# Kernel tuning notes

Measured on AMD Instinct MI355X. Metric: run time of the kernel, lower is better.

The kernel has to match this reference:

```python
import jax, jax.numpy as jnp
import numpy as np

S = 14
B = 2
L_COORD = 5.0
L_NOOBJ = 0.5
NUM_CLS = 20


def setup_inputs() -> dict:
    key = jax.random.key(0)
    k1, k2, k3, k4 = jax.random.split(key, 4)
    N = 4096
    pred_tensor = jax.random.uniform(k1, (N, S, S, B * 5 + NUM_CLS), dtype=jnp.float32)
    target_boxes = jax.random.uniform(k2, (N, S, S, 4), dtype=jnp.float32)
    target_cls = jax.random.uniform(k3, (N, S, S, NUM_CLS), dtype=jnp.float32)
    has_object_map = jax.random.randint(k4, (N, S, S), 0, 2) > 0
    return {"pred_tensor": pred_tensor, "target_boxes": target_boxes,
            "target_cls": target_cls, "has_object_map": has_object_map}


def _xywh2xyxy(b):
    # b[..., 4] in (x, y, w, h); x,y are scaled by S (grid coords)
    x, y, w, h = b[..., 0], b[..., 1], b[..., 2], b[..., 3]
    return jnp.stack([x / S - 0.5 * w, y / S - 0.5 * h,
                      x / S + 0.5 * w, y / S + 0.5 * h], axis=-1)


def reference(pred_tensor, target_boxes, target_cls, has_object_map):
    N = pred_tensor.shape[0]
    maskf = has_object_map.astype(pred_tensor.dtype)  # (N,S,S)

    # split predictions: (N,S,S,B,5) boxes and (N,S,S,20) classes
    pred_boxes = pred_tensor[..., : 5 * B].reshape(pred_tensor.shape[:3] + (B, 5))
    pred_cls = pred_tensor[..., -NUM_CLS:]

    # class loss over object cells
    cls_loss = jnp.sum(((pred_cls - target_cls) ** 2) * maskf[..., None]) / N

    # no-object confidence loss over non-object cells, all B boxes
    no_obj_loss = L_NOOBJ * jnp.sum((pred_boxes[..., 4] ** 2) * (1.0 - maskf)[..., None]) / N

    # IoU of each of the B predicted boxes vs the GT box, per cell (vectorized)
    pb = _xywh2xyxy(pred_boxes[..., :4])              # (N,S,S,B,4)
    gb = _xywh2xyxy(target_boxes)[..., None, :]        # (N,S,S,1,4)
    lt = jnp.maximum(pb[..., :2], gb[..., :2])
    rb = jnp.minimum(pb[..., 2:], gb[..., 2:])
    wh = jnp.clip(rb - lt, 0.0)
    inter = wh[..., 0] * wh[..., 1]                    # (N,S,S,B)
    area_p = (pb[..., 2] - pb[..., 0]) * (pb[..., 3] - pb[..., 1])
    area_g = (gb[..., 2] - gb[..., 0]) * (gb[..., 3] - gb[..., 1])
    iou = inter / (area_p + area_g - inter)            # (N,S,S,B)

    # per-cell best box (first-max index, matching torch.max)
    best_idx = jnp.argmax(iou, axis=-1)                # (N,S,S)
    best_boxes = jnp.take_along_axis(pred_boxes, best_idx[..., None, None], axis=3)
    best_boxes = jnp.squeeze(best_boxes, axis=3)       # (N,S,S,5)

    xy_term = jnp.sum((best_boxes[..., :2] - target_boxes[..., :2]) ** 2, axis=-1)
    wh_term = jnp.sum((jnp.sqrt(best_boxes[..., 2:4]) - jnp.sqrt(target_boxes[..., 2:4])) ** 2, axis=-1)
    reg_loss = L_COORD * jnp.sum((xy_term + wh_term) * maskf) / N

    # containing-object confidence loss: (conf - 1)^2 over object cells
    contain_conf_loss = jnp.sum(((best_boxes[..., 4] - 1.0) ** 2) * maskf) / N

    total_loss = reg_loss + contain_conf_loss + no_obj_loss + cls_loss
    return (total_loss, reg_loss, contain_conf_loss, no_obj_loss, cls_loss)
```

## Files before the change

kernel.cpp:

```cpp
#include <hip/hip_runtime.h>

#define SS 14
#define NUM_CLS 20
#define L_COORD 5.0f
#define L_NOOBJ 0.5f
#define CPB 256


__global__ void __launch_bounds__(256) yolo_main(
    const float* __restrict__ pred,
    const float* __restrict__ tbox,
    const float* __restrict__ tcls,
    const int* __restrict__ mask,
    float4* __restrict__ part) {
  __shared__ float lp[CPB * 30];
  __shared__ float lm[CPB];
  __shared__ float4 red[4];

  const int tid = threadIdx.x;
  const size_t base = (size_t)blockIdx.x * CPB;

  const float4* gc = (const float4*)(tcls + base * 20);
  float4 c0 = gc[tid];
  float4 c1 = gc[tid + 256];
  float4 c2 = gc[tid + 512];
  float4 c3 = gc[tid + 768];
  float4 c4 = gc[tid + 1024];
  float4 tb = ((const float4*)tbox)[base + tid];
  float m = mask[base + tid] ? 1.0f : 0.0f;
  lm[tid] = m;

  const float4* gp = (const float4*)(pred + base * 30);
  float4* sp = (float4*)lp;
#pragma unroll
  for (int i = 0; i < 7; ++i) sp[tid + i * 256] = gp[tid + i * 256];
  if (tid < 128) sp[tid + 1792] = gp[tid + 1792];
  __syncthreads();

  float cls_c = 0.f;
#define CLSQ(cq, i)                                          \
  {                                                          \
    int e = tid + 256 * (i);                                 \
    int cell = e / 5;                                        \
    int k = e - 5 * cell;                                    \
    const float* P = lp + cell * 30 + 10 + 4 * k;            \
    float w = lm[cell];                                      \
    float d0 = P[0] - cq.x, d1 = P[1] - cq.y;                \
    float d2 = P[2] - cq.z, d3 = P[3] - cq.w;                \
    cls_c += w * (d0 * d0 + d1 * d1 + d2 * d2 + d3 * d3);    \
  }
  CLSQ(c0, 0)
  CLSQ(c1, 1)
  CLSQ(c2, 2)
  CLSQ(c3, 3)
  CLSQ(c4, 4)
#undef CLSQ

  const float* P = lp + tid * 30;
  float p0 = P[0], p1 = P[1], p2 = P[2], p3 = P[3], p4 = P[4];
  float p5 = P[5], p6 = P[6], p7 = P[7], p8 = P[8], p9 = P[9];

  float noobj_c = (1.0f - m) * (p4 * p4 + p9 * p9);

  const float invS = 1.0f / (float)SS;
  float gx0 = tb.x * invS - 0.5f * tb.z, gy0 = tb.y * invS - 0.5f * tb.w;
  float gx1 = tb.x * invS + 0.5f * tb.z, gy1 = tb.y * invS + 0.5f * tb.w;
  float ag = (gx1 - gx0) * (gy1 - gy0);

  float iou0, iou1;
  {
    float px0 = p0 * invS - 0.5f * p2, py0 = p1 * invS - 0.5f * p3;
    float px1 = p0 * invS + 0.5f * p2, py1 = p1 * invS + 0.5f * p3;
    float lx = fmaxf(px0, gx0), ly = fmaxf(py0, gy0);
    float rx = fminf(px1, gx1), ry = fminf(py1, gy1);
    float iw = fmaxf(rx - lx, 0.f), ih = fmaxf(ry - ly, 0.f);
    float inter = iw * ih;
    float ap = (px1 - px0) * (py1 - py0);
    iou0 = inter / (ap + ag - inter);
  }
  {
    float px0 = p5 * invS - 0.5f * p7, py0 = p6 * invS - 0.5f * p8;
    float px1 = p5 * invS + 0.5f * p7, py1 = p6 * invS + 0.5f * p8;
    float lx = fmaxf(px0, gx0), ly = fmaxf(py0, gy0);
    float rx = fminf(px1, gx1), ry = fminf(py1, gy1);
    float iw = fmaxf(rx - lx, 0.f), ih = fmaxf(ry - ly, 0.f);
    float inter = iw * ih;
    float ap = (px1 - px0) * (py1 - py0);
    iou1 = inter / (ap + ag - inter);
  }
  bool pick1 = (iou1 > iou0);
  float bx = pick1 ? p5 : p0;
  float by = pick1 ? p6 : p1;
  float bw = pick1 ? p7 : p2;
  float bh = pick1 ? p8 : p3;
  float bc = pick1 ? p9 : p4;

  float dx = bx - tb.x, dy = by - tb.y;
  float dw = sqrtf(bw) - sqrtf(tb.z);
  float dh = sqrtf(bh) - sqrtf(tb.w);
  float reg_c = m * (dx * dx + dy * dy + dw * dw + dh * dh);
  float dc = bc - 1.0f;
  float con_c = m * dc * dc;

  float vx = cls_c, vy = noobj_c, vz = reg_c, vw = con_c;
  for (int off = 32; off >= 1; off >>= 1) {
    vx += __shfl_down(vx, off);
    vy += __shfl_down(vy, off);
    vz += __shfl_down(vz, off);
    vw += __shfl_down(vw, off);
  }
  int wid = tid >> 6;
  if ((tid & 63) == 0) red[wid] = make_float4(vx, vy, vz, vw);
  __syncthreads();
  if (tid == 0) {
    float4 t = red[0];
#pragma unroll
    for (int i = 1; i < 4; ++i) {
      t.x += red[i].x;
      t.y += red[i].y;
      t.z += red[i].z;
      t.w += red[i].w;
    }
    part[blockIdx.x] = t;
  }
}

__global__ void __launch_bounds__(256) yolo_reduce(
    const float4* __restrict__ part, float* __restrict__ out,
    int nblocks, float invN) {
  const int tid = threadIdx.x;
  float vx = 0.f, vy = 0.f, vz = 0.f, vw = 0.f;
  for (int i = tid; i < nblocks; i += 256) {
    float4 t = part[i];
    vx += t.x;
    vy += t.y;
    vz += t.z;
    vw += t.w;
  }
  for (int off = 32; off >= 1; off >>= 1) {
    vx += __shfl_down(vx, off);
    vy += __shfl_down(vy, off);
    vz += __shfl_down(vz, off);
    vw += __shfl_down(vw, off);
  }
  __shared__ float4 red[4];
  int wid = tid >> 6;
  if ((tid & 63) == 0) red[wid] = make_float4(vx, vy, vz, vw);
  __syncthreads();
  if (tid == 0) {
    float4 t = red[0];
#pragma unroll
    for (int i = 1; i < 4; ++i) {
      t.x += red[i].x;
      t.y += red[i].y;
      t.z += red[i].z;
      t.w += red[i].w;
    }
    float cls = t.x * invN;
    float noobj = L_NOOBJ * t.y * invN;
    float reg = L_COORD * t.z * invN;
    float con = t.w * invN;
    out[0] = reg + con + noobj + cls;
    out[1] = reg;
    out[2] = con;
    out[3] = noobj;
    out[4] = cls;
  }
}

extern "C" void kernel_launch(void* const* d_in, const int* in_sizes, int n_in,
                              void* d_out, int out_size, void* d_ws, size_t ws_size,
                              hipStream_t stream) {
  const float* pred = (const float*)d_in[0];
  const float* tbox = (const float*)d_in[1];
  const float* tcls = (const float*)d_in[2];
  const int* mask = (const int*)d_in[3];
  float* out = (float*)d_out;
  float4* part = (float4*)d_ws;

  int ncells = in_sizes[3];
  int nblocks = ncells / CPB;
  float invN = 1.0f / (float)(ncells / (SS * SS));

  yolo_main<<<nblocks, CPB, 0, stream>>>(pred, tbox, tcls, mask, part);
  yolo_reduce<<<1, 256, 0, stream>>>(part, out, nblocks, invN);
}
```

Baseline: 203.4 us.

## Load per-cell predictions directly from global memory instead of staging in LDS

Drops the shared-memory staging of the 30-float prediction rows and the class-loss redistribution. Each thread now reads its own cell's predictions (as float2) and target classes (as float4) straight from global memory and computes all loss terms locally. This removes roughly 30KB of LDS per block and a barrier, which should raise occupancy. The cost is strided, non-coalesced per-thread global loads (120-byte and 80-byte strides per lane), which rely on the caches to merge the traffic.

```diff
diff --git a/kernel.cpp b/kernel.cpp
--- a/kernel.cpp
+++ b/kernel.cpp
@@ -13,52 +13,22 @@
     const float* __restrict__ tcls,
     const int* __restrict__ mask,
     float4* __restrict__ part) {
-  __shared__ float lp[CPB * 30];
-  __shared__ float lm[CPB];
-  __shared__ float4 red[4];
+  const int tid = threadIdx.x;
+  const int c = blockIdx.x * CPB + tid;
 
-  const int tid = threadIdx.x;
-  const size_t base = (size_t)blockIdx.x * CPB;
+  const float2* p2 = (const float2*)(pred + (size_t)c * 30);
+  float2 a0 = p2[0], a1 = p2[1], a2 = p2[2], a3 = p2[3], a4 = p2[4];
+  float4 tb = ((const float4*)tbox)[c];
+  int mi = mask[c];
+  float2 b0 = p2[5], b1 = p2[6], b2 = p2[7], b3 = p2[8], b4 = p2[9];
+  float2 b5 = p2[10], b6 = p2[11], b7 = p2[12], b8 = p2[13], b9 = p2[14];
+  const float4* gc = (const float4*)(tcls + (size_t)c * 20);
+  float4 c0 = gc[0], c1 = gc[1], c2 = gc[2], c3 = gc[3], c4 = gc[4];
 
-  const float4* gc = (const float4*)(tcls + base * 20);
-  float4 c0 = gc[tid];
-  float4 c1 = gc[tid + 256];
-  float4 c2 = gc[tid + 512];
-  float4 c3 = gc[tid + 768];
-  float4 c4 = gc[tid + 1024];
-  float4 tb = ((const float4*)tbox)[base + tid];
-  float m = mask[base + tid] ? 1.0f : 0.0f;
-  lm[tid] = m;
+  float m = mi ? 1.0f : 0.0f;
 
-  const float4* gp = (const float4*)(pred + base * 30);
-  float4* sp = (float4*)lp;
-#pragma unroll
-  for (int i = 0; i < 7; ++i) sp[tid + i * 256] = gp[tid + i * 256];
-  if (tid < 128) sp[tid + 1792] = gp[tid + 1792];
-  __syncthreads();
-
-  float cls_c = 0.f;
-#define CLSQ(cq, i)                                          \
-  {                                                          \
-    int e = tid + 256 * (i);                                 \
-    int cell = e / 5;                                        \
-    int k = e - 5 * cell;                                    \
-    const float* P = lp + cell * 30 + 10 + 4 * k;            \
-    float w = lm[cell];                                      \
-    float d0 = P[0] - cq.x, d1 = P[1] - cq.y;                \
-    float d2 = P[2] - cq.z, d3 = P[3] - cq.w;                \
-    cls_c += w * (d0 * d0 + d1 * d1 + d2 * d2 + d3 * d3);    \
-  }
-  CLSQ(c0, 0)
-  CLSQ(c1, 1)
-  CLSQ(c2, 2)
-  CLSQ(c3, 3)
-  CLSQ(c4, 4)
-#undef CLSQ
-
-  const float* P = lp + tid * 30;
-  float p0 = P[0], p1 = P[1], p2 = P[2], p3 = P[3], p4 = P[4];
-  float p5 = P[5], p6 = P[6], p7 = P[7], p8 = P[8], p9 = P[9];
+  float p0 = a0.x, p1 = a0.y, p2v = a1.x, p3 = a1.y, p4 = a2.x;
+  float p5 = a2.y, p6 = a3.x, p7 = a3.y, p8 = a4.x, p9 = a4.y;
 
   float noobj_c = (1.0f - m) * (p4 * p4 + p9 * p9);
 
@@ -69,8 +39,8 @@
 
   float iou0, iou1;
   {
-    float px0 = p0 * invS - 0.5f * p2, py0 = p1 * invS - 0.5f * p3;
-    float px1 = p0 * invS + 0.5f * p2, py1 = p1 * invS + 0.5f * p3;
+    float px0 = p0 * invS - 0.5f * p2v, py0 = p1 * invS - 0.5f * p3;
+    float px1 = p0 * invS + 0.5f * p2v, py1 = p1 * invS + 0.5f * p3;
     float lx = fmaxf(px0, gx0), ly = fmaxf(py0, gy0);
     float rx = fminf(px1, gx1), ry = fminf(py1, gy1);
     float iw = fmaxf(rx - lx, 0.f), ih = fmaxf(ry - ly, 0.f);
@@ -91,7 +61,7 @@
   bool pick1 = (iou1 > iou0);
   float bx = pick1 ? p5 : p0;
   float by = pick1 ? p6 : p1;
-  float bw = pick1 ? p7 : p2;
+  float bw = pick1 ? p7 : p2v;
   float bh = pick1 ? p8 : p3;
   float bc = pick1 ? p9 : p4;
 
@@ -102,6 +72,22 @@
   float dc = bc - 1.0f;
   float con_c = m * dc * dc;
 
+  float s = 0.f;
+  {
+    float d;
+    d = b0.x - c0.x; s += d * d;  d = b0.y - c0.y; s += d * d;
+    d = b1.x - c0.z; s += d * d;  d = b1.y - c0.w; s += d * d;
+    d = b2.x - c1.x; s += d * d;  d = b2.y - c1.y; s += d * d;
+    d = b3.x - c1.z; s += d * d;  d = b3.y - c1.w; s += d * d;
+    d = b4.x - c2.x; s += d * d;  d = b4.y - c2.y; s += d * d;
+    d = b5.x - c2.z; s += d * d;  d = b5.y - c2.w; s += d * d;
+    d = b6.x - c3.x; s += d * d;  d = b6.y - c3.y; s += d * d;
+    d = b7.x - c3.z; s += d * d;  d = b7.y - c3.w; s += d * d;
+    d = b8.x - c4.x; s += d * d;  d = b8.y - c4.y; s += d * d;
+    d = b9.x - c4.z; s += d * d;  d = b9.y - c4.w; s += d * d;
+  }
+  float cls_c = s * m;
+
   float vx = cls_c, vy = noobj_c, vz = reg_c, vw = con_c;
   for (int off = 32; off >= 1; off >>= 1) {
     vx += __shfl_down(vx, off);
@@ -109,6 +95,7 @@
     vz += __shfl_down(vz, off);
     vw += __shfl_down(vw, off);
   }
+  __shared__ float4 red[4];
   int wid = tid >> 6;
   if ((tid & 63) == 0) red[wid] = make_float4(vx, vy, vz, vw);
   __syncthreads();
```

New measurement: 203.6 us. About the same (+0.1%).
